# Kernel optimization log

Hardware: AMD Instinct MI355X
Metric: run time of the kernel (lower is better)

Reference implementation:

```python
import jax, jax.numpy as jnp
import numpy as np

NUM_HEADS = 16
HEAD_DIM = 64  # hidden_size 1024 / 16 heads


def setup_inputs() -> dict:
    key = jax.random.key(0)
    k1, k2, k3, k4 = jax.random.split(key, 4)
    B, S, H = 2, 2048, 1024
    qkv = jax.random.normal(k1, (B, S, H), dtype=jnp.float32)
    # True = masked position (tf.where(mask, -inf, scores))
    mask = jax.random.bernoulli(k2, 0.5, (B, S))
    Wqkv = jax.random.normal(k3, (H, 3 * H), dtype=jnp.float32) * (H ** -0.5)
    bqkv = jnp.zeros((3 * H,), dtype=jnp.float32)
    Wo = jax.random.normal(k4, (H, H), dtype=jnp.float32) * (H ** -0.5)
    bo = jnp.zeros((H,), dtype=jnp.float32)
    return {"qkv": qkv, "mask": mask, "Wqkv": Wqkv, "bqkv": bqkv, "Wo": Wo, "bo": bo}


def reference(qkv, mask, Wqkv, bqkv, Wo, bo):
    B, S, H = qkv.shape
    nh, hd = NUM_HEADS, HEAD_DIM
    proj = qkv @ Wqkv + bqkv                       # (B,S,3H)
    q, k, v = jnp.split(proj, 3, axis=-1)
    # NOTE: original MULTIPLIES query by sqrt(head_dim) (faithful to source)
    q = q * (hd ** 0.5)
    q = q.reshape(B, S, nh, hd).transpose(0, 2, 1, 3)   # (B,h,S,d)
    k = k.reshape(B, S, nh, hd).transpose(0, 2, 1, 3)
    v = v.reshape(B, S, nh, hd).transpose(0, 2, 1, 3)
    scores = jnp.einsum("bhqd,bhkd->bhqk", q, k)        # (B,h,S,S)
    scores = jnp.where(mask[:, None, None, :], -jnp.inf, scores)
    attn = jax.nn.softmax(scores, axis=-1)              # dropout identity at inference
    out = jnp.einsum("bhqk,bhkd->bhqd", attn, v)        # (B,h,S,d)
    out = out.transpose(0, 2, 1, 3).reshape(B, S, H)
    return out @ Wo + bo
```

## Files before the change

kernel.cpp:

```cpp
#include <hip/hip_runtime.h>

#define DEV __device__ __forceinline__

typedef unsigned short u16;
typedef unsigned int u32;
typedef __attribute__((ext_vector_type(4))) float f32x4;
typedef __attribute__((ext_vector_type(8))) short s16x8;
typedef __attribute__((ext_vector_type(8))) _Float16 f16x8;
typedef __attribute__((ext_vector_type(4))) unsigned short u16x4;
typedef __attribute__((ext_vector_type(4))) unsigned int u32x4;

#define BATCH 2
#define SEQ 2048
#define HID 1024
#define NH 16
#define HD 64

#define SCALE_XW 64.0f
#define INV_PROJ (1.0f / 4096.0f)
#define SCALE_Q 46.16624130844683f
#define SCALE_K 16.0f
#define SC_TO_LOG2 0.015625f
#define DEFER_THR 10.0f

DEV f32x4 mfmah(s16x8 a, s16x8 b, f32x4 c) {
    return __builtin_amdgcn_mfma_f32_16x16x32_f16(
        __builtin_bit_cast(f16x8, a), __builtin_bit_cast(f16x8, b), c, 0, 0, 0);
}

DEV u16 f2h(float x) { return __builtin_bit_cast(u16, (_Float16)x); }
DEV float h2f(u16 h) { return (float)__builtin_bit_cast(_Float16, h); }

DEV u32 pkh(float a, float b) {
#if __has_builtin(__builtin_amdgcn_cvt_pkrtz)
    auto r = __builtin_amdgcn_cvt_pkrtz(a, b);
    return __builtin_bit_cast(u32, r);
#else
    return (u32)f2h(a) | ((u32)f2h(b) << 16);
#endif
}

DEV float fexp2(float x) {
#if __has_builtin(__builtin_amdgcn_exp2f)
    return __builtin_amdgcn_exp2f(x);
#else
    return exp2f(x);
#endif
}

DEV void swap32(int lane, u32 a, u32 b, u32& o0, u32& o1) {
#if __has_builtin(__builtin_amdgcn_permlane32_swap)
    auto r = __builtin_amdgcn_permlane32_swap((int)a, (int)b, false, false);
    o0 = (u32)r[0]; o1 = (u32)r[1];
#else
    u32 ax = (u32)__shfl_xor((int)a, 32);
    u32 bx = (u32)__shfl_xor((int)b, 32);
    bool hi = (lane & 32) != 0;
    o0 = hi ? bx : a;
    o1 = hi ? b : ax;
#endif
}
DEV void swap16(int lane, u32 a, u32 b, u32& o0, u32& o1) {
#if __has_builtin(__builtin_amdgcn_permlane16_swap)
    auto r = __builtin_amdgcn_permlane16_swap((int)a, (int)b, false, false);
    o0 = (u32)r[0]; o1 = (u32)r[1];
#else
    u32 ax = (u32)__shfl_xor((int)a, 16);
    u32 bx = (u32)__shfl_xor((int)b, 16);
    bool hi = (lane & 16) != 0;
    o0 = hi ? bx : a;
    o1 = hi ? b : ax;
#endif
}

DEV void gl_lds16(const void* g, void* l) {
    __builtin_amdgcn_global_load_lds(
        (__attribute__((address_space(1))) void*)(void*)g,
        (__attribute__((address_space(3))) void*)l, 16, 0, 0);
}

DEV void vm0_bar() {
    __builtin_amdgcn_sched_barrier(0);
    asm volatile("s_waitcnt vmcnt(0)" ::: "memory");
    __builtin_amdgcn_s_barrier();
    __builtin_amdgcn_sched_barrier(0);
}

DEV s16x8 lds_ld16(const u16* base, int row, int kbyte) {
    return *(const s16x8*)((const char*)base + row * 128 + (kbyte ^ ((row & 7) << 4)));
}
DEV s16x8 lds_ld32r(const u16* base, int row, int g) {
    return *(const s16x8*)((const char*)base + row * 64 + ((g * 16) ^ ((row & 3) << 4)));
}

__global__ void detect_mask(const unsigned char* __restrict__ m, float* __restrict__ pbias,
                            int* __restrict__ pack_idx, int* __restrict__ cnt) {
    __shared__ int sb, sf;
    __shared__ int scan[256];
    int tid = threadIdx.x;
    if (tid == 0) { sb = 0; sf = 0; }
    __syncthreads();
    int lb = 0, lf = 0;
    for (int i = tid * 16; i < tid * 16 + 16; i++) {
        unsigned char v = m[i];
        int pos = i & 3;
        if (pos == 3 && v == 0x3f) lf = 1;
        if (pos != 0 && v != 0) lb = 1;
    }
    if (lb) atomicOr(&sb, 1);
    if (lf) atomicOr(&sf, 1);
    __syncthreads();
    int f = sf ? 2 : (sb ? 1 : 0);
#pragma unroll
    for (int b = 0; b < BATCH; b++) {
        int base = b * SEQ;
        int keep[8], lc = 0;
#pragma unroll
        for (int e = 0; e < 8; e++) {
            int i = base + tid * 8 + e;
            int mv;
            if (f == 0) mv = ((const int*)m)[i] != 0;
            else if (f == 1) mv = m[i] != 0;
            else mv = ((const float*)m)[i] != 0.0f;
            keep[e] = !mv;
            lc += keep[e];
        }
        scan[tid] = lc;
        __syncthreads();
        for (int s = 1; s < 256; s <<= 1) {
            int v = (tid >= s) ? scan[tid - s] : 0;
            __syncthreads();
            scan[tid] += v;
            __syncthreads();
        }
        int off = scan[tid] - lc;
        int total = scan[255];
        __syncthreads();
#pragma unroll
        for (int e = 0; e < 8; e++)
            if (keep[e]) pack_idx[base + off++] = base + tid * 8 + e;
        if (tid == 0) cnt[b] = total;
        for (int j = tid; j < SEQ; j += 256)
            pbias[base + j] = (j < total) ? 0.0f : -1e30f;
    }
}

__global__ __launch_bounds__(256) void split_x(const float* __restrict__ in,
                                               u16* __restrict__ oh) {
    int i = (blockIdx.x * 256 + threadIdx.x) * 4;
    f32x4 v = *(const f32x4*)&in[i];
    u16x4 h;
#pragma unroll
    for (int e = 0; e < 4; e++) h[e] = f2h(v[e] * SCALE_XW);
    *(u16x4*)&oh[i] = h;
}

__global__ __launch_bounds__(256) void transpose_split(const float* __restrict__ in,
                                                       u16* __restrict__ oh,
                                                       int K, int N, float scale) {
    __shared__ float t[32][33];
    int tx = threadIdx.x, ty = threadIdx.y;
    int n0 = blockIdx.x * 32, k0 = blockIdx.y * 32;
#pragma unroll
    for (int i = 0; i < 4; i++)
        t[ty + 8 * i][tx] = in[(size_t)(k0 + ty + 8 * i) * N + n0 + tx];
    __syncthreads();
#pragma unroll
    for (int i = 0; i < 4; i++) {
        float v = t[tx][ty + 8 * i] * scale;
        size_t o = (size_t)(n0 + ty + 8 * i) * K + k0 + tx;
        oh[o] = f2h(v);
    }
}

__global__ __launch_bounds__(256, 3) void gemm_qkv(
    const u16* __restrict__ Xh,
    const u16* __restrict__ Wth,
    const float* __restrict__ bqkv,
    const int* __restrict__ pack_idx, const int* __restrict__ cnt,
    u16* __restrict__ qh,
    u16* __restrict__ kh,
    u16* __restrict__ vt) {
    __shared__ __align__(16) u16 SM[2][128 * 32];
    __shared__ __align__(16) u16 T[64 * 140];
    int tid = threadIdx.x, lane = tid & 63, w = tid >> 6;
    int g = lane >> 4, q15 = lane & 15;
    int wm = w >> 1, wn = w & 1;
    int m0 = blockIdx.y * 128, n0 = blockIdx.x * 128;
    int part = n0 >> 10;
    int bb = m0 >> 11;
    int cb = cnt[bb];
    if (part != 0 && (m0 & 2047) >= cb) return;

    int srcrow[2];
#pragma unroll
    for (int i = 0; i < 2; i++) {
        int r = m0 + ((i * 256 + tid) >> 2);
        srcrow[i] = (part == 0) ? r : (((r & 2047) < cb) ? pack_idx[r] : (bb << 11));
    }

    f32x4 acc[4][4];
#pragma unroll
    for (int i = 0; i < 4; i++)
#pragma unroll
        for (int j = 0; j < 4; j++) acc[i][j] = (f32x4){0.f, 0.f, 0.f, 0.f};

    auto STAGE = [&](int kt) {
        int k0 = kt * 32;
#pragma unroll
        for (int i = 0; i < 2; i++) {
            int c = i * 256 + tid;
            int row = c >> 2, slot = c & 3;
            int sg = slot ^ (row & 3);
            int dst = (c & ~63) * 8;
            size_t ga = (size_t)srcrow[i] * 1024 + k0 + sg * 8;
            size_t gb = (size_t)(n0 + row) * 1024 + k0 + sg * 8;
            gl_lds16(&Xh[ga], &SM[0][dst]);
            gl_lds16(&Wth[gb], &SM[1][dst]);
        }
    };

    STAGE(0);
    for (int kt = 0; kt < 32; kt++) {
        vm0_bar();
        s16x8 a_h[4], b_h[4];
#pragma unroll
        for (int i = 0; i < 4; i++) {
            a_h[i] = lds_ld32r(SM[0], wm * 64 + i * 16 + q15, g);
            b_h[i] = lds_ld32r(SM[1], wn * 64 + i * 16 + q15, g);
        }
        __syncthreads();
        if (kt < 31) STAGE(kt + 1);
#pragma unroll
        for (int mi = 0; mi < 4; mi++)
#pragma unroll
            for (int ni = 0; ni < 4; ni++)
                acc[mi][ni] = mfmah(a_h[mi], b_h[ni], acc[mi][ni]);
    }

    if (part == 2) {
        const int TP = 140;
#pragma unroll
        for (int h2 = 0; h2 < 2; h2++) {
            __syncthreads();
            if (wn == h2) {
#pragma unroll
                for (int mi = 0; mi < 4; mi++)
#pragma unroll
                    for (int ni = 0; ni < 4; ni++) {
                        int lcol = ni * 16 + q15;
#pragma unroll
                        for (int j = 0; j < 4; j++) {
                            int lrow = wm * 64 + mi * 16 + g * 4 + j;
                            T[lcol * TP + lrow] =
                                f2h(acc[mi][ni][j] * INV_PROJ + bqkv[n0 + h2 * 64 + lcol]);
                        }
                    }
            }
            __syncthreads();
            int lcol = tid >> 2;
            int seg = tid & 3;
            int c = n0 - 2048 + h2 * 64 + lcol;
            int h = c >> 6, d = c & 63;
            int b = m0 >> 11, sbase = m0 & 2047;
            size_t rowbase = ((size_t)(b * NH + h) * HD + d) * SEQ + sbase;
#pragma unroll
            for (int k = 0; k < 2; k++) {
                int slot = seg * 2 + k;
                *(s16x8*)&vt[rowbase + slot * 16 + 0] = *(const s16x8*)&T[lcol * TP + slot * 16 + 0];
                *(s16x8*)&vt[rowbase + slot * 16 + 8] = *(const s16x8*)&T[lcol * TP + slot * 16 + 8];
            }
        }
    } else {
#pragma unroll
        for (int mi = 0; mi < 4; mi++)
#pragma unroll
            for (int ni = 0; ni < 4; ni++) {
                int col = n0 + wn * 64 + ni * 16 + q15;
                float bias = bqkv[col];
                int cc = col & 1023, h = cc >> 6, d = cc & 63;
#pragma unroll
                for (int j = 0; j < 4; j++) {
                    int row = m0 + wm * 64 + mi * 16 + g * 4 + j;
                    int b = row >> 11, s = row & 2047;
                    float v = acc[mi][ni][j] * INV_PROJ + bias;
                    v *= (part == 0) ? SCALE_Q : SCALE_K;
                    size_t o = (size_t)(b * NH + h) * SEQ * HD + (size_t)s * HD + d;
                    if (part == 0) qh[o] = f2h(v);
                    else kh[o] = f2h(v);
                }
            }
    }
}

__global__ __launch_bounds__(256, 4) void attn_kernel(
    const u16* __restrict__ qh,
    const u16* __restrict__ kh,
    const u16* __restrict__ vt, const float* __restrict__ pbias,
    const int* __restrict__ cnt,
    u16* __restrict__ att) {
    __shared__ __align__(16) u16 Kh[2][4096], Vt[2][4096];
    __shared__ __align__(16) float MskB[2][64];
    int tid = threadIdx.x, lane = tid & 63, w = tid >> 6;
    int g = lane >> 4, q15 = lane & 15;
    int bid = blockIdx.y * 32 + blockIdx.x;
    int swz = (bid & 7) * 128 + (bid >> 3);
    int qt = swz & 31, bh = swz >> 5;
    int b = bh >> 4, h = bh & 15;
    int q0 = qt * 64;
    int NT = (cnt[b] + 63) >> 6;
    size_t base = (size_t)bh * SEQ * HD;
    const u16* vbase = vt + (size_t)bh * HD * SEQ;
    const float* mrow = pbias + b * SEQ;

    s16x8 aq[2];
#pragma unroll
    for (int k2 = 0; k2 < 2; k2++) {
        size_t o = base + (size_t)(q0 + w * 16 + q15) * HD + k2 * 32 + g * 8;
        aq[k2] = *(const s16x8*)&qh[o];
    }

    float m_ = -1e30f, l_ = 0.f;
    f32x4 o_[4];
#pragma unroll
    for (int df = 0; df < 4; df++) o_[df] = (f32x4){0.f, 0.f, 0.f, 0.f};

    auto STAGE = [&](int buf, int k0) {
#pragma unroll
        for (int i = 0; i < 2; i++) {
            int c = i * 256 + tid;
            int row = c >> 3, slot = c & 7;
            int sg = slot ^ (row & 7);
            int dst = (c & ~63) * 8;
            size_t gK = base + (size_t)(k0 + row) * HD + sg * 8;
            gl_lds16(&kh[gK], &Kh[buf][dst]);
            size_t gV = (size_t)row * SEQ + k0 + sg * 8;
            gl_lds16(&vbase[gV], &Vt[buf][dst]);
        }
        if (tid < 16) gl_lds16(&mrow[k0 + tid * 4], &MskB[buf][0]);
    };

    STAGE(0, 0);
    __syncthreads();

    for (int kt = 0; kt < NT; kt++) {
        int cur = kt & 1;
        if (kt < NT - 1) STAGE(cur ^ 1, (kt + 1) * 64);

        f32x4 sc[4];
#pragma unroll
        for (int nf = 0; nf < 4; nf++) sc[nf] = (f32x4){0.f, 0.f, 0.f, 0.f};
#pragma unroll
        for (int nf = 0; nf < 4; nf++) {
#pragma unroll
            for (int k2 = 0; k2 < 2; k2++) {
                int kb = k2 * 64 + g * 16;
                s16x8 kbh = lds_ld16(Kh[cur], nf * 16 + q15, kb);
                sc[nf] = mfmah(kbh, aq[k2], sc[nf]);
            }
            f32x4 mb = *(const f32x4*)&MskB[cur][nf * 16 + g * 4];
            sc[nf] = sc[nf] * SC_TO_LOG2 + mb;
        }

        float pml = -1e30f;
#pragma unroll
        for (int nf = 0; nf < 4; nf++)
#pragma unroll
            for (int j = 0; j < 4; j++) pml = fmaxf(pml, sc[nf][j]);
        if (!__all(pml - m_ <= DEFER_THR)) {
            float pm = fmaxf(pml, __shfl_xor(pml, 16));
            pm = fmaxf(pm, __shfl_xor(pm, 32));
            float mn = fmaxf(m_, pm);
            float scl = fexp2(m_ - mn);
            m_ = mn;
            l_ *= scl;
#pragma unroll
            for (int j = 0; j < 4; j++) {
                float sb = __shfl(scl, g * 4 + j);
#pragma unroll
                for (int df = 0; df < 4; df++) o_[df][j] *= sb;
            }
        }
        float p[4][4];
        float rs = 0.f;
#pragma unroll
        for (int nf = 0; nf < 4; nf++)
#pragma unroll
            for (int j = 0; j < 4; j++) {
                float pv = fexp2(sc[nf][j] - m_);
                p[nf][j] = pv;
                rs += pv;
            }
        l_ += rs;
        s16x8 pa[2];
#pragma unroll
        for (int k2 = 0; k2 < 2; k2++) {
            u32 A0 = pkh(p[2 * k2][0], p[2 * k2][1]);
            u32 A1 = pkh(p[2 * k2][2], p[2 * k2][3]);
            u32 B0 = pkh(p[2 * k2 + 1][0], p[2 * k2 + 1][1]);
            u32 B1 = pkh(p[2 * k2 + 1][2], p[2 * k2 + 1][3]);
            u32 s0, s1, t0, t1, w0, w1, w2, w3;
            swap32(lane, A0, B0, s0, s1);
            swap16(lane, s0, s1, w0, w2);
            swap32(lane, A1, B1, t0, t1);
            swap16(lane, t0, t1, w1, w3);
            u32x4 words = {w0, w1, w2, w3};
            pa[k2] = __builtin_bit_cast(s16x8, words);
        }

#pragma unroll
        for (int k2 = 0; k2 < 2; k2++) {
            int kb = k2 * 64 + g * 16;
#pragma unroll
            for (int df = 0; df < 4; df++) {
                s16x8 vb = lds_ld16(Vt[cur], df * 16 + q15, kb);
                o_[df] = mfmah(pa[k2], vb, o_[df]);
            }
        }
        __syncthreads();
    }

    float lt = l_;
    lt += __shfl_xor(lt, 16);
    lt += __shfl_xor(lt, 32);
#pragma unroll
    for (int j = 0; j < 4; j++) {
        float lb = __shfl(lt, g * 4 + j);
        float linv = __builtin_amdgcn_rcpf(lb);
        int qrow = q0 + w * 16 + g * 4 + j;
        size_t srow = (size_t)(b * SEQ + qrow);
#pragma unroll
        for (int df = 0; df < 4; df++) {
            int col = h * HD + df * 16 + q15;
            att[srow * HID + col] = f2h(o_[df][j] * linv);
        }
    }
}

__global__ __launch_bounds__(256, 4) void gemm_out(
    const u16* __restrict__ A, const u16* __restrict__ Bh0,
    const float* __restrict__ bo, float* __restrict__ out) {
    __shared__ __align__(16) u16 SMa[2][64 * 32], SMb[2][128 * 32];
    int tid = threadIdx.x, lane = tid & 63, w = tid >> 6;
    int g = lane >> 4, q15 = lane & 15;
    int wm = w >> 1, wn = w & 1;
    int m0 = blockIdx.y * 64, n0 = blockIdx.x * 128;
    f32x4 acc[2][4];
#pragma unroll
    for (int i = 0; i < 2; i++)
#pragma unroll
        for (int j = 0; j < 4; j++) acc[i][j] = (f32x4){0.f, 0.f, 0.f, 0.f};

    auto STAGE = [&](int db, int kt) {
        int k0 = kt * 32;
        {
            int c = tid;
            int row = c >> 2, slot = c & 3;
            int sg = slot ^ (row & 3);
            int dst = (c & ~63) * 8;
            gl_lds16(&A[(size_t)(m0 + row) * 1024 + k0 + sg * 8], &SMa[db][dst]);
        }
#pragma unroll
        for (int i = 0; i < 2; i++) {
            int c = i * 256 + tid;
            int row = c >> 2, slot = c & 3;
            int sg = slot ^ (row & 3);
            int dst = (c & ~63) * 8;
            gl_lds16(&Bh0[(size_t)(n0 + row) * 1024 + k0 + sg * 8], &SMb[db][dst]);
        }
    };

    STAGE(0, 0);
    for (int kt = 0; kt < 32; kt++) {
        int cur = kt & 1;
        __syncthreads();
        if (kt < 31) STAGE(cur ^ 1, kt + 1);
        s16x8 a_[2], b_[4];
#pragma unroll
        for (int i = 0; i < 2; i++)
            a_[i] = lds_ld32r(SMa[cur], wm * 32 + i * 16 + q15, g);
#pragma unroll
        for (int i = 0; i < 4; i++)
            b_[i] = lds_ld32r(SMb[cur], wn * 64 + i * 16 + q15, g);
#pragma unroll
        for (int mi = 0; mi < 2; mi++)
#pragma unroll
            for (int ni = 0; ni < 4; ni++)
                acc[mi][ni] = mfmah(a_[mi], b_[ni], acc[mi][ni]);
    }
#pragma unroll
    for (int mi = 0; mi < 2; mi++)
#pragma unroll
        for (int ni = 0; ni < 4; ni++) {
            int col = n0 + wn * 64 + ni * 16 + q15;
            float bias = bo[col];
#pragma unroll
            for (int j = 0; j < 4; j++) {
                int row = m0 + wm * 32 + mi * 16 + g * 4 + j;
                out[(size_t)row * 1024 + col] = acc[mi][ni][j] + bias;
            }
        }
}

extern "C" void kernel_launch(void* const* d_in, const int* in_sizes, int n_in,
                              void* d_out, int out_size, void* d_ws, size_t ws_size,
                              hipStream_t stream) {
    const float* qkv = (const float*)d_in[0];
    const void* mask = d_in[1];
    const float* Wqkv = (const float*)d_in[2];
    const float* bqkv = (const float*)d_in[3];
    const float* Wo = (const float*)d_in[4];
    const float* bo = (const float*)d_in[5];
    float* out = (float*)d_out;

    const size_t SZ_X = (size_t)4096 * 1024 * 2;
    const size_t SZ_W = (size_t)3072 * 1024 * 2;
    const size_t SZ_WO = (size_t)1024 * 1024 * 2;
    const size_t SZ_QKV = (size_t)32 * 2048 * 64 * 2;
    const size_t SZ_ATT = (size_t)4096 * 1024 * 2;

    char* p = (char*)d_ws;
    u16* Xh = (u16*)p; p += SZ_X;
    u16* Wth = (u16*)p; p += SZ_W;
    u16* Woth = (u16*)p; p += SZ_WO;
    u16* qh = (u16*)p; p += SZ_QKV;
    u16* kh = (u16*)p; p += SZ_QKV;
    u16* vt = (u16*)p; p += SZ_QKV;
    u16* att = (u16*)p; p += SZ_ATT;
    float* pbias = (float*)p; p += BATCH * SEQ * 4;
    int* pack_idx = (int*)p; p += BATCH * SEQ * 4;
    int* cnt = (int*)p; p += 256;

    detect_mask<<<1, 256, 0, stream>>>((const unsigned char*)mask, pbias, pack_idx, cnt);
    split_x<<<4096, 256, 0, stream>>>(qkv, Xh);
    transpose_split<<<dim3(96, 32), dim3(32, 8), 0, stream>>>(Wqkv, Wth, 1024, 3072, SCALE_XW);
    transpose_split<<<dim3(32, 32), dim3(32, 8), 0, stream>>>(Wo, Woth, 1024, 1024, 1.0f);
    gemm_qkv<<<dim3(24, 32), 256, 0, stream>>>(Xh, Wth, bqkv, pack_idx, cnt, qh, kh, vt);
    attn_kernel<<<dim3(32, 32), 256, 0, stream>>>(qh, kh, vt, pbias, cnt, att);
    gemm_out<<<dim3(8, 64), 256, 0, stream>>>(att, Woth, bo, out);
}
```

Baseline: 110.2 us.

## Double query rows per attention block to reuse staged K/V tiles

Each attention workgroup now handles 128 query rows instead of 64, with each wave owning two 16-row groups that share every K and V fragment read from LDS. The grid is halved and the block swizzle adjusted to match. This halves global-to-LDS staging of K/V and the LDS fragment reads per MFMA, at the cost of more registers (launch bounds lowered to 2) and fewer blocks, which means less occupancy and less parallelism across the 1024-tile grid.

New measurement: 109.9 us. No clear change (-0.3%).

```diff
diff --git a/kernel.cpp b/kernel.cpp
--- a/kernel.cpp
+++ b/kernel.cpp
@@ -293,7 +293,7 @@
     }
 }
 
-__global__ __launch_bounds__(256, 4) void attn_kernel(
+__global__ __launch_bounds__(256, 2) void attn_kernel(
     const u16* __restrict__ qh,
     const u16* __restrict__ kh,
     const u16* __restrict__ vt, const float* __restrict__ pbias,
@@ -303,27 +303,31 @@
     __shared__ __align__(16) float MskB[2][64];
     int tid = threadIdx.x, lane = tid & 63, w = tid >> 6;
     int g = lane >> 4, q15 = lane & 15;
-    int bid = blockIdx.y * 32 + blockIdx.x;
-    int swz = (bid & 7) * 128 + (bid >> 3);
-    int qt = swz & 31, bh = swz >> 5;
+    int bid = blockIdx.y * 16 + blockIdx.x;
+    int swz = (bid & 7) * 64 + (bid >> 3);
+    int qt = swz & 15, bh = swz >> 4;
     int b = bh >> 4, h = bh & 15;
-    int q0 = qt * 64;
+    int q0 = qt * 128;
     int NT = (cnt[b] + 63) >> 6;
     size_t base = (size_t)bh * SEQ * HD;
     const u16* vbase = vt + (size_t)bh * HD * SEQ;
     const float* mrow = pbias + b * SEQ;
 
-    s16x8 aq[2];
-#pragma unroll
-    for (int k2 = 0; k2 < 2; k2++) {
-        size_t o = base + (size_t)(q0 + w * 16 + q15) * HD + k2 * 32 + g * 8;
-        aq[k2] = *(const s16x8*)&qh[o];
-    }
-
-    float m_ = -1e30f, l_ = 0.f;
-    f32x4 o_[4];
-#pragma unroll
-    for (int df = 0; df < 4; df++) o_[df] = (f32x4){0.f, 0.f, 0.f, 0.f};
+    s16x8 aq[2][2];
+#pragma unroll
+    for (int grp = 0; grp < 2; grp++)
+#pragma unroll
+        for (int k2 = 0; k2 < 2; k2++) {
+            size_t o = base + (size_t)(q0 + w * 32 + grp * 16 + q15) * HD + k2 * 32 + g * 8;
+            aq[grp][k2] = *(const s16x8*)&qh[o];
+        }
+
+    float m_[2] = {-1e30f, -1e30f}, l_[2] = {0.f, 0.f};
+    f32x4 o_[2][4];
+#pragma unroll
+    for (int grp = 0; grp < 2; grp++)
+#pragma unroll
+        for (int df = 0; df < 4; df++) o_[grp][df] = (f32x4){0.f, 0.f, 0.f, 0.f};
 
     auto STAGE = [&](int buf, int k0) {
 #pragma unroll
@@ -347,65 +351,74 @@
         int cur = kt & 1;
         if (kt < NT - 1) STAGE(cur ^ 1, (kt + 1) * 64);
 
-        f32x4 sc[4];
-#pragma unroll
-        for (int nf = 0; nf < 4; nf++) sc[nf] = (f32x4){0.f, 0.f, 0.f, 0.f};
+        f32x4 sc0[4], sc1[4];
+#pragma unroll
+        for (int nf = 0; nf < 4; nf++) {
+            sc0[nf] = (f32x4){0.f, 0.f, 0.f, 0.f};
+            sc1[nf] = (f32x4){0.f, 0.f, 0.f, 0.f};
+        }
 #pragma unroll
         for (int nf = 0; nf < 4; nf++) {
 #pragma unroll
             for (int k2 = 0; k2 < 2; k2++) {
                 int kb = k2 * 64 + g * 16;
                 s16x8 kbh = lds_ld16(Kh[cur], nf * 16 + q15, kb);
-                sc[nf] = mfmah(kbh, aq[k2], sc[nf]);
+                sc0[nf] = mfmah(kbh, aq[0][k2], sc0[nf]);
+                sc1[nf] = mfmah(kbh, aq[1][k2], sc1[nf]);
             }
             f32x4 mb = *(const f32x4*)&MskB[cur][nf * 16 + g * 4];
-            sc[nf] = sc[nf] * SC_TO_LOG2 + mb;
-        }
-
-        float pml = -1e30f;
-#pragma unroll
-        for (int nf = 0; nf < 4; nf++)
-#pragma unroll
-            for (int j = 0; j < 4; j++) pml = fmaxf(pml, sc[nf][j]);
-        if (!__all(pml - m_ <= DEFER_THR)) {
-            float pm = fmaxf(pml, __shfl_xor(pml, 16));
-            pm = fmaxf(pm, __shfl_xor(pm, 32));
-            float mn = fmaxf(m_, pm);
-            float scl = fexp2(m_ - mn);
-            m_ = mn;
-            l_ *= scl;
-#pragma unroll
-            for (int j = 0; j < 4; j++) {
-                float sb = __shfl(scl, g * 4 + j);
-#pragma unroll
-                for (int df = 0; df < 4; df++) o_[df][j] *= sb;
-            }
-        }
-        float p[4][4];
-        float rs = 0.f;
-#pragma unroll
-        for (int nf = 0; nf < 4; nf++)
-#pragma unroll
-            for (int j = 0; j < 4; j++) {
-                float pv = fexp2(sc[nf][j] - m_);
-                p[nf][j] = pv;
-                rs += pv;
-            }
-        l_ += rs;
-        s16x8 pa[2];
-#pragma unroll
-        for (int k2 = 0; k2 < 2; k2++) {
-            u32 A0 = pkh(p[2 * k2][0], p[2 * k2][1]);
-            u32 A1 = pkh(p[2 * k2][2], p[2 * k2][3]);
-            u32 B0 = pkh(p[2 * k2 + 1][0], p[2 * k2 + 1][1]);
-            u32 B1 = pkh(p[2 * k2 + 1][2], p[2 * k2 + 1][3]);
-            u32 s0, s1, t0, t1, w0, w1, w2, w3;
-            swap32(lane, A0, B0, s0, s1);
-            swap16(lane, s0, s1, w0, w2);
-            swap32(lane, A1, B1, t0, t1);
-            swap16(lane, t0, t1, w1, w3);
-            u32x4 words = {w0, w1, w2, w3};
-            pa[k2] = __builtin_bit_cast(s16x8, words);
+            sc0[nf] = sc0[nf] * SC_TO_LOG2 + mb;
+            sc1[nf] = sc1[nf] * SC_TO_LOG2 + mb;
+        }
+
+        s16x8 pa[2][2];
+#pragma unroll
+        for (int grp = 0; grp < 2; grp++) {
+            f32x4* sc = grp ? sc1 : sc0;
+            float pml = -1e30f;
+#pragma unroll
+            for (int nf = 0; nf < 4; nf++)
+#pragma unroll
+                for (int j = 0; j < 4; j++) pml = fmaxf(pml, sc[nf][j]);
+            if (!__all(pml - m_[grp] <= DEFER_THR)) {
+                float pm = fmaxf(pml, __shfl_xor(pml, 16));
+                pm = fmaxf(pm, __shfl_xor(pm, 32));
+                float mn = fmaxf(m_[grp], pm);
+                float scl = fexp2(m_[grp] - mn);
+                m_[grp] = mn;
+                l_[grp] *= scl;
+#pragma unroll
+                for (int j = 0; j < 4; j++) {
+                    float sb = __shfl(scl, g * 4 + j);
+#pragma unroll
+                    for (int df = 0; df < 4; df++) o_[grp][df][j] *= sb;
+                }
+            }
+            float p[4][4];
+            float rs = 0.f;
+#pragma unroll
+            for (int nf = 0; nf < 4; nf++)
+#pragma unroll
+                for (int j = 0; j < 4; j++) {
+                    float pv = fexp2(sc[nf][j] - m_[grp]);
+                    p[nf][j] = pv;
+                    rs += pv;
+                }
+            l_[grp] += rs;
+#pragma unroll
+            for (int k2 = 0; k2 < 2; k2++) {
+                u32 A0 = pkh(p[2 * k2][0], p[2 * k2][1]);
+                u32 A1 = pkh(p[2 * k2][2], p[2 * k2][3]);
+                u32 B0 = pkh(p[2 * k2 + 1][0], p[2 * k2 + 1][1]);
+                u32 B1 = pkh(p[2 * k2 + 1][2], p[2 * k2 + 1][3]);
+                u32 s0, s1, t0, t1, w0, w1, w2, w3;
+                swap32(lane, A0, B0, s0, s1);
+                swap16(lane, s0, s1, w0, w2);
+                swap32(lane, A1, B1, t0, t1);
+                swap16(lane, t0, t1, w1, w3);
+                u32x4 words = {w0, w1, w2, w3};
+                pa[grp][k2] = __builtin_bit_cast(s16x8, words);
+            }
         }
 
 #pragma unroll
@@ -414,25 +427,29 @@
 #pragma unroll
             for (int df = 0; df < 4; df++) {
                 s16x8 vb = lds_ld16(Vt[cur], df * 16 + q15, kb);
-                o_[df] = mfmah(pa[k2], vb, o_[df]);
+                o_[0][df] = mfmah(pa[0][k2], vb, o_[0][df]);
+                o_[1][df] = mfmah(pa[1][k2], vb, o_[1][df]);
             }
         }
         __syncthreads();
     }
 
-    float lt = l_;
-    lt += __shfl_xor(lt, 16);
-    lt += __shfl_xor(lt, 32);
-#pragma unroll
-    for (int j = 0; j < 4; j++) {
-        float lb = __shfl(lt, g * 4 + j);
-        float linv = __builtin_amdgcn_rcpf(lb);
-        int qrow = q0 + w * 16 + g * 4 + j;
-        size_t srow = (size_t)(b * SEQ + qrow);
-#pragma unroll
-        for (int df = 0; df < 4; df++) {
-            int col = h * HD + df * 16 + q15;
-            att[srow * HID + col] = f2h(o_[df][j] * linv);
+#pragma unroll
+    for (int grp = 0; grp < 2; grp++) {
+        float lt = l_[grp];
+        lt += __shfl_xor(lt, 16);
+        lt += __shfl_xor(lt, 32);
+#pragma unroll
+        for (int j = 0; j < 4; j++) {
+            float lb = __shfl(lt, g * 4 + j);
+            float linv = __builtin_amdgcn_rcpf(lb);
+            int qrow = q0 + w * 32 + grp * 16 + g * 4 + j;
+            size_t srow = (size_t)(b * SEQ + qrow);
+#pragma unroll
+            for (int df = 0; df < 4; df++) {
+                int col = h * HD + df * 16 + q15;
+                att[srow * HID + col] = f2h(o_[grp][df][j] * linv);
+            }
         }
     }
 }
@@ -536,6 +553,6 @@
     transpose_split<<<dim3(96, 32), dim3(32, 8), 0, stream>>>(Wqkv, Wth, 1024, 3072, SCALE_XW);
     transpose_split<<<dim3(32, 32), dim3(32, 8), 0, stream>>>(Wo, Woth, 1024, 1024, 1.0f);
     gemm_qkv<<<dim3(24, 32), 256, 0, stream>>>(Xh, Wth, bqkv, pack_idx, cnt, qh, kh, vt);
-    attn_kernel<<<dim3(32, 32), 256, 0, stream>>>(qh, kh, vt, pbias, cnt, att);
+    attn_kernel<<<dim3(16, 32), 256, 0, stream>>>(qh, kh, vt, pbias, cnt, att);
     gemm_out<<<dim3(8, 64), 256, 0, stream>>>(att, Woth, bo, out);
 }
```
